# Optimization experiments

Measured on AMD Instinct MI355X. Metric: run time of the kernel, lower is better.

Reference implementation:

```python
import jax, jax.numpy as jnp
from jax import lax
import numpy as np

B, L, NW, D, KS, TOPK, H = 32, 16384, 8000, 10, 22, 50, 2  # batch, seqlen, vocab, dim, conv kernel, top-k, heads
DN = ('NHWC', 'HWIO', 'NHWC')


def setup_inputs() -> dict:
    key = jax.random.key(0)
    ks = jax.random.split(key, 20)
    def n(i, shape, s=0.05):
        return jax.random.normal(ks[i], shape, jnp.float32) * s
    # tokens in [1, NW] -> no padding, so the ragged per-sample path is a dense batch
    inputs = jax.random.randint(ks[0], (B, 2, L), 1, NW + 1, dtype=jnp.int32)
    return {
        'inputs': inputs,
        'emb': n(1, (NW + 1, D), 0.1),            # Embedding(n_words+1, dim)
        'w1': n(2, (KS, KS, 1, 1)), 'b1': jnp.zeros((1,), jnp.float32),
        'w2': n(3, (KS, KS, 1, 1)), 'b2': jnp.zeros((1,), jnp.float32),
        'w3': n(4, (KS, KS, 1, 1)), 'b3': jnp.zeros((1,), jnp.float32),
        'wq': n(5, (D, H, D), 0.2), 'bq': jnp.zeros((H, D), jnp.float32),
        'wk': n(6, (D, H, D), 0.2), 'bk': jnp.zeros((H, D), jnp.float32),
        'wv': n(7, (D, H, D), 0.2), 'bv': jnp.zeros((H, D), jnp.float32),
        'wo': n(8, (H, D, D), 0.2), 'bo': jnp.zeros((D,), jnp.float32),
        'wf': n(9, (D, 2), 0.3), 'bf': jnp.zeros((2,), jnp.float32),
    }


def _encode(tok, emb, convs):
    x = emb[tok][..., None]                      # [B, L, D, 1] (NHWC, H=L, W=D)
    for w, b in convs:
        x = jax.nn.relu(lax.conv_general_dilated(x, w, (1, 1), 'SAME', dimension_numbers=DN) + b)
    x = jnp.transpose(x[..., 0], (0, 2, 1))      # [B, D, L]
    x = lax.top_k(x, TOPK)[0]                    # top-50 activations per channel
    return jnp.transpose(x, (0, 2, 1))           # [B, 50, D]


def _mha(q, kv, wq, bq, wk, bk, wv, bv, wo, bo):
    # keras MultiHeadAttention(num_heads=2, key_dim=D), key defaults to value
    Q = jnp.einsum('bqd,dhe->bqhe', q, wq) + bq
    K = jnp.einsum('bsd,dhe->bshe', kv, wk) + bk
    V = jnp.einsum('bsd,dhe->bshe', kv, wv) + bv
    logits = jnp.einsum('bqhe,bshe->bhqs', Q, K) / jnp.sqrt(jnp.float32(D))
    A = jax.nn.softmax(logits, axis=-1)
    O = jnp.einsum('bhqs,bshe->bqhe', A, V)
    return jnp.einsum('bqhe,hed->bqd', O, wo) + bo


def reference(inputs, emb, w1, b1, w2, b2, w3, b3, wq, bq, wk, bk, wv, bv, wo, bo, wf, bf):
    convs = ((w1, b1), (w2, b2), (w3, b3))
    f1 = _encode(inputs[:, 0], emb, convs)       # [B, 50, D]
    f2 = _encode(inputs[:, 1], emb, convs)
    r1 = jnp.sum(_mha(f1, f2, wq, bq, wk, bk, wv, bv, wo, bo), axis=1)  # [B, D]
    r2 = jnp.sum(_mha(f2, f1, wq, bq, wk, bk, wv, bv, wo, bo), axis=1)
    x = jnp.stack([r1, r2], axis=1)              # [B, 2, D]  (Concatenate axis=2 on [B,1,1,D])
    out = jax.nn.softmax(x @ wf + bf, axis=-1)   # [B, 2, 2]
    return out.reshape(-1, 2)                    # [2B, 2]
```

## Files before the change

kernel.cpp:

```cpp
#include <hip/hip_runtime.h>
#include <hip/hip_bf16.h>

#define LSEQ   16384
#define BATCH  32
#define NBS    64
#define NW     8000
#define CHUNK  448
#define NCHK   37
#define ROWS   536
#define RS     24

typedef short v8s __attribute__((ext_vector_type(8)));
typedef float v4f __attribute__((ext_vector_type(4)));
typedef _Float16 hf2 __attribute__((ext_vector_type(2)));

__device__ __forceinline__ unsigned short f2bf(float f) {
  unsigned u = __float_as_uint(f);
  unsigned r = u + 0x7FFFu + ((u >> 16) & 1u);
  return (unsigned short)(r >> 16);
}
__device__ __forceinline__ unsigned short cvt_bf16(float v) {
  __hip_bfloat16 hb = __float2bfloat16(v);
  unsigned short us;
  __builtin_memcpy(&us, &hb, 2);
  return us;
}

__global__ __launch_bounds__(256) void prep_kernel(
    const float* __restrict__ emb, const float* __restrict__ w1,
    const float* __restrict__ w2, const float* __restrict__ w3,
    unsigned short* __restrict__ emb16, unsigned short* __restrict__ bh) {
  int bid = blockIdx.x;
  if (bid < 32) {
    int r = bid * 256 + threadIdx.x;
    if (r > NW) return;
    const float2* er = reinterpret_cast<const float2*>(emb + r * 10);
    float v[10];
#pragma unroll
    for (int k = 0; k < 5; ++k) { float2 t2 = er[k]; v[2 * k] = t2.x; v[2 * k + 1] = t2.y; }
    v8s lo8 = (v8s)0, hi8 = (v8s)0;
#pragma unroll
    for (int j = 0; j < 8; ++j) lo8[j] = (short)f2bf(v[j]);
    hi8[0] = (short)f2bf(v[8]);
    hi8[1] = (short)f2bf(v[9]);
    v8s* dst = reinterpret_cast<v8s*>(emb16 + r * 16);
    dst[0] = lo8;
    dst[1] = hi8;
  } else {
    int idx = (bid - 32) * 256 + threadIdx.x;
    if (idx >= 3 * 11 * 64) return;
    int lane = idx & 63, rest = idx >> 6;
    int t = rest % 11, stage = rest / 11;
    const float* W = (stage == 0) ? w1 : (stage == 1) ? w2 : w3;
    int col = lane & 15;
    int kh = 2 * t + (lane >> 5);
    int wi0 = ((lane >> 4) & 1) * 8;
#pragma unroll
    for (int j = 0; j < 8; ++j) {
      int wi = wi0 + j;
      int kw = wi - col + 10;
      float v = (wi < 10 && col < 10 && kw >= 0 && kw < 22) ? W[kh * 22 + kw] : 0.0f;
      bh[idx * 8 + j] = f2bf(v);
    }
  }
}

__device__ __forceinline__ unsigned h2max_u(unsigned a, unsigned b) {
  hf2 r = __builtin_elementwise_max(__builtin_bit_cast(hf2, a),
                                    __builtin_bit_cast(hf2, b));
  return __builtin_bit_cast(unsigned, r);
}
__device__ __forceinline__ unsigned h2min_u(unsigned a, unsigned b) {
  hf2 r = __builtin_elementwise_min(__builtin_bit_cast(hf2, a),
                                    __builtin_bit_cast(hf2, b));
  return __builtin_bit_cast(unsigned, r);
}
__device__ __forceinline__ unsigned bsort64_h2(unsigned v, int lane) {
#pragma unroll
  for (int k = 2; k <= 64; k <<= 1) {
#pragma unroll
    for (int j = k >> 1; j > 0; j >>= 1) {
      unsigned o = __shfl_xor(v, j, 64);
      bool keepmax = (((lane & k) == 0) == ((lane & j) == 0));
      unsigned mx = h2max_u(v, o), mn = h2min_u(v, o);
      v = keepmax ? mx : mn;
    }
  }
  return v;
}
__device__ __forceinline__ unsigned bmerge64_h2(unsigned a, unsigned b, int lane) {
  unsigned rb = __shfl(b, 63 - lane, 64);
  unsigned m = h2max_u(a, rb);
#pragma unroll
  for (int j = 32; j > 0; j >>= 1) {
    unsigned o = __shfl_xor(m, j, 64);
    unsigned mx = h2max_u(m, o), mn = h2min_u(m, o);
    m = ((lane & j) == 0) ? mx : mn;
  }
  return m;
}

__global__ __launch_bounds__(512, 6) void conv_fused_kernel(
    const int* __restrict__ inputs, const unsigned short* __restrict__ emb16,
    const float* __restrict__ b1, const float* __restrict__ b2,
    const float* __restrict__ b3,
    const unsigned short* __restrict__ bh,
    unsigned* __restrict__ candp ) {
  __shared__ unsigned short plane[ROWS * RS];

  int blk = blockIdx.x;
  int bs = blk / NCHK;
  int chunk = blk - bs * NCHK;
  int base = chunk * CHUNK;
  int tid = threadIdx.x;
  int lane = tid & 63, wave = tid >> 6;

  const int* tokp = inputs + bs * LSEQ;
  for (int i = tid; i < ROWS; i += 512) {
    int seq = base - 32 + i;
    v8s lo8 = (v8s)0, hi8 = (v8s)0;
    if ((unsigned)seq < (unsigned)LSEQ) {
      int tok = tokp[seq];
      const v8s* er = reinterpret_cast<const v8s*>(emb16 + tok * 16);
      lo8 = er[0];
      hi8 = er[1];
    }
    *reinterpret_cast<v8s*>(&plane[i * RS + 0]) = lo8;
    *reinterpret_cast<v8s*>(&plane[i * RS + 8]) = hi8;
  }
  __syncthreads();

  const int laneA = ((lane & 15) + (lane >> 5) + 22) * RS + ((lane >> 4) & 1) * 8;
  const int col = lane & 15;
  const int rbase = (lane >> 4) * 4;

#pragma unroll 1
  for (int stage = 0; stage < 3; ++stage) {
    const int lo = (stage == 0) ? -20 : (stage == 1) ? -10 : 0;
    const int ntiles = (stage == 0) ? 32 : (stage == 1) ? 30 : 28;
    const float bias = (stage == 0) ? b1[0] : (stage == 1) ? b2[0] : b3[0];
    const int nt = (ntiles - wave + 7) >> 3;

    v4f acc[4];
#pragma unroll
    for (int m = 0; m < 4; ++m)
#pragma unroll
      for (int j = 0; j < 4; ++j) acc[m][j] = 0.0f;

    const v8s* bhf = reinterpret_cast<const v8s*>(bh) + (stage * 11) * 64 + lane;
    v8s bhc = bhf[0];

#pragma unroll 1
    for (int t = 0; t < 11; ++t) {
      v8s bhn = bhc;
      if (t < 10) bhn = bhf[(t + 1) * 64];
      const int toff = laneA + t * 2 * RS;
#pragma unroll
      for (int m = 0; m < 4; ++m) {
        if (m < nt) {
          int r0 = lo + (wave + 8 * m) * 16;
          v8s a = *reinterpret_cast<const v8s*>(&plane[toff + r0 * RS]);
          acc[m] = __builtin_amdgcn_mfma_f32_16x16x32_bf16(a, bhc, acc[m], 0, 0, 0);
        }
      }
      bhc = bhn;
    }
    __syncthreads();

#pragma unroll
    for (int m = 0; m < 4; ++m) {
      if (m < nt) {
        int r0 = lo + (wave + 8 * m) * 16;
#pragma unroll
        for (int j = 0; j < 4; ++j) {
          int rloc = r0 + rbase + j;
          int seq = base + rloc;
          unsigned short us = cvt_bf16(fmaxf(acc[m][j] + bias, 0.0f));
          bool ok = (col < 10) && ((unsigned)seq < (unsigned)LSEQ);
          plane[(rloc + 32) * RS + col] = ok ? us : (unsigned short)0;
        }
      }
    }
    __syncthreads();
  }

  if (wave < 5) {
    int p = wave;
    unsigned x[7];
#pragma unroll
    for (int s = 0; s < 7; ++s) {
      unsigned w = *reinterpret_cast<const unsigned*>(
          &plane[(32 + s * 64 + lane) * RS + 2 * p]);
      float flo = __uint_as_float(w << 16);
      float fhi = __uint_as_float(w & 0xFFFF0000u);
      hf2 h;
      h[0] = (_Float16)flo;
      h[1] = (_Float16)fhi;
      x[s] = __builtin_bit_cast(unsigned, h);
    }
#pragma unroll
    for (int s = 0; s < 7; ++s) x[s] = bsort64_h2(x[s], lane);
    unsigned y0 = bmerge64_h2(x[0], x[1], lane);
    unsigned y1 = bmerge64_h2(x[2], x[3], lane);
    unsigned y2 = bmerge64_h2(x[4], x[5], lane);
    unsigned z0 = bmerge64_h2(y0, y1, lane);
    unsigned z1 = bmerge64_h2(y2, x[6], lane);
    unsigned t  = bmerge64_h2(z0, z1, lane);
    if (lane < 50)
      candp[((bs * 5 + p) * NCHK + chunk) * 50 + lane] = t;
  }
}

__global__ __launch_bounds__(256) void mha_kernel(
    const unsigned* __restrict__ candp,
    const float* __restrict__ wq, const float* __restrict__ bq,
    const float* __restrict__ wk, const float* __restrict__ bk,
    const float* __restrict__ wv, const float* __restrict__ bv,
    const float* __restrict__ wo, const float* __restrict__ bo,
    const float* __restrict__ wf, const float* __restrict__ bf,
    float* __restrict__ out) {
  __shared__ float f[2][50][10];
  __shared__ float Qm[50][2][10];
  __shared__ float Km[50][2][10];
  __shared__ float Vm[50][2][10];
  __shared__ float A2[2][50][50];
  __shared__ float Abar[2][50];
  __shared__ float OS[2][10];
  __shared__ float rr[10];

  int blk = blockIdx.x, b = blk >> 1, dir = blk & 1;
  int qs = dir, ks = dir ^ 1;
  int tid = threadIdx.x;
  int lane = tid & 63, wave = tid >> 6;

  for (int s = wave; s < 10; s += 4) {
    int s2 = s / 5, p = s - s2 * 5;
    int bs = 2 * b + s2;
    const unsigned* src = candp + ((bs * 5 + p) * NCHK) * 50;
    unsigned v[NCHK];
    if (lane < 50) {
#pragma unroll
      for (int c = 0; c < NCHK; ++c) v[c] = src[c * 50 + lane];
    } else {
#pragma unroll
      for (int c = 0; c < NCHK; ++c) v[c] = 0u;
    }
    unsigned acc = v[0];
#pragma unroll
    for (int c = 1; c < NCHK; ++c)
      acc = bmerge64_h2(acc, v[c], lane);
    if (lane < 50) {
      hf2 h = __builtin_bit_cast(hf2, acc);
      f[s2][lane][2 * p + 0] = (float)h[0];
      f[s2][lane][2 * p + 1] = (float)h[1];
    }
  }
  __syncthreads();

  for (int i = tid; i < 1000; i += 256) {
    int q = i / 20, rem = i - q * 20;
    int h = rem / 10, e = rem - h * 10;
    const float* fq = f[qs][q];
    const float* fk = f[ks][q];
    float aq = bq[h * 10 + e], ak = bk[h * 10 + e], av = bv[h * 10 + e];
#pragma unroll
    for (int dd = 0; dd < 10; ++dd) {
      int wIdx = dd * 20 + h * 10 + e;
      aq = fmaf(fq[dd], wq[wIdx], aq);
      ak = fmaf(fk[dd], wk[wIdx], ak);
      av = fmaf(fk[dd], wv[wIdx], av);
    }
    Qm[q][h][e] = aq; Km[q][h][e] = ak; Vm[q][h][e] = av;
  }
  __syncthreads();

  for (int row = tid; row < 100; row += 256) {
    int h = row / 50, q = row - h * 50;
    const float* Qr = Qm[q][h];
    float lg[50], m = -1e30f;
#pragma unroll
    for (int s = 0; s < 50; ++s) {
      const float* Kr = Km[s][h];
      float t = 0.0f;
#pragma unroll
      for (int e = 0; e < 10; ++e) t = fmaf(Qr[e], Kr[e], t);
      t *= 0.31622776601683794f;
      lg[s] = t; m = fmaxf(m, t);
    }
    float sum = 0.0f;
#pragma unroll
    for (int s = 0; s < 50; ++s) { float p = __expf(lg[s] - m); lg[s] = p; sum += p; }
    float inv = 1.0f / sum;
#pragma unroll
    for (int s = 0; s < 50; ++s) A2[h][q][s] = lg[s] * inv;
  }
  __syncthreads();

  for (int i = tid; i < 100; i += 256) {
    int h = i / 50, s = i - h * 50;
    float t = 0.0f;
#pragma unroll
    for (int q = 0; q < 50; ++q) t += A2[h][q][s];
    Abar[h][s] = t;
  }
  __syncthreads();
  if (tid < 20) {
    int h = tid / 10, e = tid - h * 10;
    float t = 0.0f;
#pragma unroll
    for (int s = 0; s < 50; ++s) t += Abar[h][s] * Vm[s][h][e];
    OS[h][e] = t;
  }
  __syncthreads();
  if (tid < 10) {
    int dc = tid;
    float t = 50.0f * bo[dc];
#pragma unroll
    for (int h = 0; h < 2; ++h)
#pragma unroll
      for (int e = 0; e < 10; ++e) t = fmaf(OS[h][e], wo[h * 100 + e * 10 + dc], t);
    rr[dc] = t;
  }
  __syncthreads();
  if (tid == 0) {
    float l0 = bf[0], l1 = bf[1];
#pragma unroll
    for (int dd = 0; dd < 10; ++dd) {
      l0 = fmaf(rr[dd], wf[dd * 2 + 0], l0);
      l1 = fmaf(rr[dd], wf[dd * 2 + 1], l1);
    }
    float m = fmaxf(l0, l1);
    float e0 = expf(l0 - m), e1 = expf(l1 - m);
    float inv = 1.0f / (e0 + e1);
    out[(b * 2 + dir) * 2 + 0] = e0 * inv;
    out[(b * 2 + dir) * 2 + 1] = e1 * inv;
  }
}

extern "C" void kernel_launch(void* const* d_in, const int* in_sizes, int n_in,
                              void* d_out, int out_size, void* d_ws, size_t ws_size,
                              hipStream_t stream) {
  const int*   inputs = (const int*)d_in[0];
  const float* emb = (const float*)d_in[1];
  const float* w1 = (const float*)d_in[2];
  const float* b1 = (const float*)d_in[3];
  const float* w2 = (const float*)d_in[4];
  const float* b2 = (const float*)d_in[5];
  const float* w3 = (const float*)d_in[6];
  const float* b3 = (const float*)d_in[7];
  const float* wq = (const float*)d_in[8];
  const float* bq = (const float*)d_in[9];
  const float* wk = (const float*)d_in[10];
  const float* bk = (const float*)d_in[11];
  const float* wv = (const float*)d_in[12];
  const float* bv = (const float*)d_in[13];
  const float* wo = (const float*)d_in[14];
  const float* bo = (const float*)d_in[15];
  const float* wf = (const float*)d_in[16];
  const float* bf = (const float*)d_in[17];
  float* out = (float*)d_out;

  unsigned* candp = (unsigned*)((float*)d_ws + 32768);
  unsigned short* bh = (unsigned short*)((float*)d_ws + 1216768);
  unsigned short* emb16 = bh + 16896;

  hipLaunchKernelGGL(prep_kernel, dim3(41), dim3(256), 0, stream,
                     emb, w1, w2, w3, emb16, bh);
  hipLaunchKernelGGL(conv_fused_kernel, dim3(NBS * NCHK), dim3(512), 0, stream,
                     inputs, emb16, b1, b2, b3, bh, candp);
  hipLaunchKernelGGL(mha_kernel, dim3(NBS), dim3(256), 0, stream,
                     candp, wq, bq, wk, bk, wv, bv, wo, bo, wf, bf, out);
}
```

Before: 115.2 us.

## Split conv LDS plane into lo/hi column planes and re-tile MFMA K dimension

The conv activation plane in shared memory is split into a dense 8-column plane and a 4-column plane instead of one 24-stride padded row layout. The weight tiles are rebuilt so each MFMA covers four kernel rows of either the low 8 or the high 2 columns, giving 12 MFMA steps per stage instead of 11. The aim is to cut LDS footprint from padding, which can raise occupancy and reduce bank conflicts. In exchange it issues one extra MFMA per tile, the high-plane steps duplicate a 4-wide load and mostly multiply zeros, and the writeback gains a branch.

```diff
diff --git a/kernel.cpp b/kernel.cpp
--- a/kernel.cpp
+++ b/kernel.cpp
@@ -7,10 +7,11 @@
 #define NW     8000
 #define CHUNK  448
 #define NCHK   37
-#define ROWS   536
-#define RS     24
+#define ROWS   538
+#define NT12   12
 
 typedef short v8s __attribute__((ext_vector_type(8)));
+typedef short v4s __attribute__((ext_vector_type(4)));
 typedef float v4f __attribute__((ext_vector_type(4)));
 typedef _Float16 hf2 __attribute__((ext_vector_type(2)));
 
@@ -48,18 +49,19 @@
     dst[1] = hi8;
   } else {
     int idx = (bid - 32) * 256 + threadIdx.x;
-    if (idx >= 3 * 11 * 64) return;
+    if (idx >= 3 * NT12 * 64) return;
     int lane = idx & 63, rest = idx >> 6;
-    int t = rest % 11, stage = rest / 11;
+    int t = rest % NT12, stage = rest / NT12;
     const float* W = (stage == 0) ? w1 : (stage == 1) ? w2 : w3;
     int col = lane & 15;
-    int kh = 2 * t + (lane >> 5);
-    int wi0 = ((lane >> 4) & 1) * 8;
+    int g = lane >> 4;
 #pragma unroll
     for (int j = 0; j < 8; ++j) {
-      int wi = wi0 + j;
+      int kh = (t < 6) ? (4 * t + g) : (4 * (t - 6) + g);
+      int wi = (t < 6) ? j : (8 + j);
       int kw = wi - col + 10;
-      float v = (wi < 10 && col < 10 && kw >= 0 && kw < 22) ? W[kh * 22 + kw] : 0.0f;
+      float v = (wi < 10 && col < 10 && kh < 22 && kw >= 0 && kw < 22)
+                    ? W[kh * 22 + kw] : 0.0f;
       bh[idx * 8 + j] = f2bf(v);
     }
   }
@@ -106,7 +108,8 @@
     const float* __restrict__ b3,
     const unsigned short* __restrict__ bh,
     unsigned* __restrict__ candp ) {
-  __shared__ unsigned short plane[ROWS * RS];
+  __shared__ unsigned short loP[ROWS * 8];
+  __shared__ unsigned short hiP[ROWS * 4];
 
   int blk = blockIdx.x;
   int bs = blk / NCHK;
@@ -118,19 +121,19 @@
   const int* tokp = inputs + bs * LSEQ;
   for (int i = tid; i < ROWS; i += 512) {
     int seq = base - 32 + i;
-    v8s lo8 = (v8s)0, hi8 = (v8s)0;
+    v8s lo8 = (v8s)0;
+    v4s h4 = (v4s)0;
     if ((unsigned)seq < (unsigned)LSEQ) {
       int tok = tokp[seq];
-      const v8s* er = reinterpret_cast<const v8s*>(emb16 + tok * 16);
-      lo8 = er[0];
-      hi8 = er[1];
-    }
-    *reinterpret_cast<v8s*>(&plane[i * RS + 0]) = lo8;
-    *reinterpret_cast<v8s*>(&plane[i * RS + 8]) = hi8;
-  }
-  __syncthreads();
-
-  const int laneA = ((lane & 15) + (lane >> 5) + 22) * RS + ((lane >> 4) & 1) * 8;
+      lo8 = *reinterpret_cast<const v8s*>(emb16 + tok * 16);
+      h4 = *reinterpret_cast<const v4s*>(emb16 + tok * 16 + 8);
+    }
+    *reinterpret_cast<v8s*>(&loP[i * 8]) = lo8;
+    *reinterpret_cast<v4s*>(&hiP[i * 4]) = h4;
+  }
+  __syncthreads();
+
+  const int rowBase = (lane & 15) + (lane >> 4) + 22;
   const int col = lane & 15;
   const int rbase = (lane >> 4) * 4;
 
@@ -147,20 +150,33 @@
 #pragma unroll
       for (int j = 0; j < 4; ++j) acc[m][j] = 0.0f;
 
-    const v8s* bhf = reinterpret_cast<const v8s*>(bh) + (stage * 11) * 64 + lane;
+    const v8s* bhf = reinterpret_cast<const v8s*>(bh) + (stage * NT12) * 64 + lane;
     v8s bhc = bhf[0];
 
 #pragma unroll 1
-    for (int t = 0; t < 11; ++t) {
+    for (int t = 0; t < NT12; ++t) {
       v8s bhn = bhc;
-      if (t < 10) bhn = bhf[(t + 1) * 64];
-      const int toff = laneA + t * 2 * RS;
-#pragma unroll
-      for (int m = 0; m < 4; ++m) {
-        if (m < nt) {
-          int r0 = lo + (wave + 8 * m) * 16;
-          v8s a = *reinterpret_cast<const v8s*>(&plane[toff + r0 * RS]);
-          acc[m] = __builtin_amdgcn_mfma_f32_16x16x32_bf16(a, bhc, acc[m], 0, 0, 0);
+      if (t < NT12 - 1) bhn = bhf[(t + 1) * 64];
+      if (t < 6) {
+        const int toff = (rowBase + 4 * t) * 8;
+#pragma unroll
+        for (int m = 0; m < 4; ++m) {
+          if (m < nt) {
+            int r0 = lo + (wave + 8 * m) * 16;
+            v8s a = *reinterpret_cast<const v8s*>(&loP[toff + r0 * 8]);
+            acc[m] = __builtin_amdgcn_mfma_f32_16x16x32_bf16(a, bhc, acc[m], 0, 0, 0);
+          }
+        }
+      } else {
+        const int toff = (rowBase + 4 * (t - 6)) * 4;
+#pragma unroll
+        for (int m = 0; m < 4; ++m) {
+          if (m < nt) {
+            int r0 = lo + (wave + 8 * m) * 16;
+            v4s h = *reinterpret_cast<const v4s*>(&hiP[toff + r0 * 4]);
+            v8s a = __builtin_shufflevector(h, h, 0, 1, 2, 3, 0, 1, 2, 3);
+            acc[m] = __builtin_amdgcn_mfma_f32_16x16x32_bf16(a, bhc, acc[m], 0, 0, 0);
+          }
         }
       }
       bhc = bhn;
@@ -177,7 +193,11 @@
           int seq = base + rloc;
           unsigned short us = cvt_bf16(fmaxf(acc[m][j] + bias, 0.0f));
           bool ok = (col < 10) && ((unsigned)seq < (unsigned)LSEQ);
-          plane[(rloc + 32) * RS + col] = ok ? us : (unsigned short)0;
+          unsigned short w = ok ? us : (unsigned short)0;
+          if (col < 8)
+            loP[(rloc + 32) * 8 + col] = w;
+          else if (col < 10)
+            hiP[(rloc + 32) * 4 + (col - 8)] = w;
         }
       }
     }
@@ -189,8 +209,10 @@
     unsigned x[7];
 #pragma unroll
     for (int s = 0; s < 7; ++s) {
-      unsigned w = *reinterpret_cast<const unsigned*>(
-          &plane[(32 + s * 64 + lane) * RS + 2 * p]);
+      int row = 32 + s * 64 + lane;
+      unsigned w = (p < 4)
+          ? *reinterpret_cast<const unsigned*>(&loP[row * 8 + 2 * p])
+          : *reinterpret_cast<const unsigned*>(&hiP[row * 4]);
       float flo = __uint_as_float(w << 16);
       float fhi = __uint_as_float(w & 0xFFFF0000u);
       hf2 h;
@@ -362,7 +384,7 @@
 
   unsigned* candp = (unsigned*)((float*)d_ws + 32768);
   unsigned short* bh = (unsigned short*)((float*)d_ws + 1216768);
-  unsigned short* emb16 = bh + 16896;
+  unsigned short* emb16 = bh + 18432;
 
   hipLaunchKernelGGL(prep_kernel, dim3(41), dim3(256), 0, stream,
                      emb, w1, w2, w3, emb16, bh);
```

New measurement: 127.5 us. 1.11x slower.
